# Performance work log

Measured on AMD Instinct MI355X. Metric: run time of the kernel, lower is better.

The kernel has to match this reference:

```python
import jax, jax.numpy as jnp
import numpy as np

EMB = 384
HID = 256
HEADS = 4
HD = HID // HEADS  # 64
LAYERS = 2
M_DOCS = 32
TOTAL = 4096  # 1 query + 32 docs + 4063 sentences
LN_EPS = 1e-5


def _layernorm(x, scale, bias):
    mu = jnp.mean(x, axis=-1, keepdims=True)
    var = jnp.mean(jnp.square(x - mu), axis=-1, keepdims=True)
    return (x - mu) * jax.lax.rsqrt(var + LN_EPS) * scale + bias


def setup_inputs() -> dict:
    key = jax.random.key(0)
    ks = jax.random.split(key, 12)
    g = 0.05  # small init scale (stand-in for xavier)
    return {
        "node_embeddings": jax.random.normal(ks[0], (TOTAL, EMB), jnp.float32),
        "adj": jax.random.randint(ks[1], (TOTAL, TOTAL), 0, 2, jnp.int32),
        "num_docs": M_DOCS,
        "proj_w": jax.random.normal(ks[2], (HID, EMB), jnp.float32) * g,
        "proj_b": jnp.zeros((HID,), jnp.float32),
        "ln_scale": jnp.ones((LAYERS, HID), jnp.float32),
        "ln_bias": jnp.zeros((LAYERS, HID), jnp.float32),
        "gat_W": jax.random.normal(ks[3], (LAYERS, HEADS, HD, HID), jnp.float32) * g,
        "gat_a": jax.random.normal(ks[4], (LAYERS, HEADS, 2 * HD), jnp.float32) * g,
        "fusion_w": jax.random.normal(ks[5], (HID, 2 * HID + 2), jnp.float32) * g,
        "fusion_b": jnp.zeros((HID,), jnp.float32),
        "out_w": jax.random.normal(ks[6], (HID,), jnp.float32) * g,
        "out_b": jnp.float32(0.5),
    }


def reference(node_embeddings, adj, num_docs, proj_w, proj_b, ln_scale, ln_bias,
              gat_W, gat_a, fusion_w, fusion_b, out_w, out_b):
    T = node_embeddings.shape[0]
    M = num_docs
    N = T - 1 - M  # number of sentences
    # input projection + relu (dropout = identity in eval)
    h = jax.nn.relu(node_embeddings @ proj_w.T + proj_b)  # (T, HID)
    # query-guided sentence re-weighting
    q = h[0:1]                     # (1, HID)
    s = h[1 + M:]                  # (N, HID)
    qn = q / (jnp.linalg.norm(q, axis=1, keepdims=True) + 1e-8)
    sn = s / (jnp.linalg.norm(s, axis=1, keepdims=True) + 1e-8)
    cos = (qn @ sn.T).reshape(-1, 1)          # (N,1)
    s = s + 0.8 * q * cos
    h = jnp.concatenate([h[:1 + M], s], axis=0)
    mask = (adj == 0)[None]                   # (1,T,T)
    for i in range(LAYERS):
        res = h
        x = _layernorm(h, ln_scale[i], ln_bias[i])
        Wh = jnp.einsum('nd,hkd->hnk', x, gat_W[i])                # (H,T,HD)
        # concat-attention a.[Wh_i ; Wh_j] == a_src.Wh_i + a_dst.Wh_j
        src = jnp.einsum('hnk,hk->hn', Wh, gat_a[i, :, :HD])       # (H,T)
        dst = jnp.einsum('hnk,hk->hn', Wh, gat_a[i, :, HD:])       # (H,T)
        e = jax.nn.leaky_relu(src[:, :, None] + dst[:, None, :], 0.2)  # (H,T,T)
        e = jnp.where(mask, -jnp.inf, e)
        attn = jax.nn.softmax(e, axis=-1)                          # softmax over j
        hn = jnp.einsum('hij,hjk->hik', attn, Wh)                  # (H,T,HD)
        hcat = jnp.transpose(hn, (1, 0, 2)).reshape(T, HEADS * HD)
        h = 0.5 * jax.nn.relu(hcat) + 0.5 * res
    qh = h[0:1]
    sh = h[1 + M:]
    scores = (qh @ sh.T) / (HID ** 0.5)       # (1,N)
    aw = jax.nn.softmax(scores, axis=-1)
    awT = aw.T                                # (N,1)
    qw = qh * (awT + 0.5)                     # (N,HID)
    qnf = qh / (jnp.linalg.norm(qh, axis=1, keepdims=True) + 1e-8)
    snf = sh / (jnp.linalg.norm(sh, axis=1, keepdims=True) + 1e-8)
    cosf = (qnf @ snf.T).reshape(-1, 1)       # (N,1)
    feat = jnp.concatenate([sh, qw, cosf, awT], axis=1)  # (N, 2*HID+2)
    g = jax.nn.relu(feat @ fusion_w.T + fusion_b)
    out = g @ out_w + out_b                   # (N,)
    return out + 0.5 * cosf[:, 0]
```

## Files before the change

kernel.cpp:

```cpp
#include <hip/hip_runtime.h>
#include <hip/hip_bf16.h>
#include <stdint.h>

#define TOTAL 4096
#define EMB 384
#define MD 32
#define NDOCS (TOTAL - 1 - MD)
#define LN_EPS 1e-5f

typedef __hip_bfloat16 bf16;
typedef unsigned short ushort_t;
typedef __attribute__((ext_vector_type(8))) short short8;
typedef __attribute__((ext_vector_type(4))) float f32x4;
typedef __attribute__((ext_vector_type(2))) float f32x2;

__device__ __forceinline__ float ldf(const void* p, int i, int isbf) {
    return isbf ? __bfloat162float(((const bf16*)p)[i]) : ((const float*)p)[i];
}

__device__ __forceinline__ ushort_t f2bf(float x) {
    return (ushort_t)((__float_as_uint(x) + 0x8000u) >> 16);
}

__global__ void k_detect(const uint16_t* p, int* flag) {
    __shared__ int red[4];
    int t = threadIdx.x;
    int cnt = 0;
    for (int k = t; k < 4096; k += 256) {
        uint16_t w = p[2 * k];
        int e = (w >> 7) & 0xFF;
        if (e >= 100 && e <= 140) cnt++;
    }
    for (int o = 32; o > 0; o >>= 1) cnt += __shfl_down(cnt, o);
    if ((t & 63) == 0) red[t >> 6] = cnt;
    __syncthreads();
    if (t == 0) flag[0] = (red[0] + red[1] + red[2] + red[3] > 2048) ? 1 : 0;
}

__global__ void k_transpose(const void* proj_w, const void* gat_W, const void* fusion_w,
                            float* projT, float* gatT, float* fwT, const int* flagp) {
    int isbf = flagp[0];
    int idx = blockIdx.x * 256 + threadIdx.x;
    if (idx < EMB * 256) {
        int d = idx >> 8, c = idx & 255;
        projT[idx] = ldf(proj_w, c * EMB + d, isbf);
    } else if (idx < EMB * 256 + 2 * 256 * 256) {
        int r = idx - EMB * 256;
        int l = r >> 16; int rem = r & 65535;
        int d = rem >> 8, c = rem & 255;
        gatT[r] = ldf(gat_W, l * 65536 + c * 256 + d, isbf);
    } else if (idx < EMB * 256 + 2 * 256 * 256 + 514 * 256) {
        int r = idx - (EMB * 256 + 2 * 256 * 256);
        int j = r >> 8, c = r & 255;
        fwT[r] = ldf(fusion_w, c * 514 + j, isbf);
    }
}

__global__ void k_adjmask(const int* adj, unsigned long long* maskb) {
    int i = blockIdx.x;
    int t = threadIdx.x;
    int w = t >> 6, l = t & 63;
    for (int c = w; c < 64; c += 4) {
        int a = adj[(size_t)i * TOTAL + c * 64 + l];
        unsigned long long m = __ballot(a != 0);
        if (l == 0) maskb[i * 64 + c] = m;
    }
}

#define PR 8
__global__ void k_proj(const void* emb, const void* proj_b, const float* projT, float* h,
                       const int* flagp) {
    __shared__ float xs[PR][EMB];
    int isbf = flagp[0];
    int i0 = blockIdx.x * PR, t = threadIdx.x;
    for (int idx = t; idx < PR * EMB; idx += 256) {
        int r = idx / EMB, d = idx % EMB;
        xs[r][d] = ldf(emb, (i0 + r) * EMB + d, isbf);
    }
    __syncthreads();
    float acc[PR];
    float bias = ldf(proj_b, t, isbf);
#pragma unroll
    for (int r = 0; r < PR; r++) acc[r] = bias;
    for (int d0 = 0; d0 < EMB; d0 += 4) {
        float w0 = projT[d0 * 256 + t];
        float w1 = projT[(d0 + 1) * 256 + t];
        float w2 = projT[(d0 + 2) * 256 + t];
        float w3 = projT[(d0 + 3) * 256 + t];
#pragma unroll
        for (int r = 0; r < PR; r++) {
            float4 x = *(const float4*)&xs[r][d0];
            acc[r] = fmaf(x.x, w0, acc[r]);
            acc[r] = fmaf(x.y, w1, acc[r]);
            acc[r] = fmaf(x.z, w2, acc[r]);
            acc[r] = fmaf(x.w, w3, acc[r]);
        }
    }
#pragma unroll
    for (int r = 0; r < PR; r++) h[(size_t)(i0 + r) * 256 + t] = fmaxf(acc[r], 0.f);
}

__global__ __launch_bounds__(256) void k_cosupdate(float* h) {
    int t = threadIdx.x, W = t >> 6, lane = t & 63;
    float4* h4 = (float4*)h;
    float4 q4 = h4[lane];
    float a = q4.x * q4.x + q4.y * q4.y + q4.z * q4.z + q4.w * q4.w;
    for (int o = 32; o > 0; o >>= 1) a += __shfl_xor(a, o);
    float qn = sqrtf(a) + 1e-8f;
    int gw = blockIdx.x * 4 + W;
    for (int n = gw; n < NDOCS; n += 1024) {
        size_t ro = (size_t)(1 + MD + n) * 64;
        float4 s4 = h4[ro + lane];
        float b = s4.x * s4.x + s4.y * s4.y + s4.z * s4.z + s4.w * s4.w;
        float c = q4.x * s4.x + q4.y * s4.y + q4.z * s4.z + q4.w * s4.w;
        for (int o = 32; o > 0; o >>= 1) { b += __shfl_xor(b, o); c += __shfl_xor(c, o); }
        float k = 0.8f * (c / (qn * (sqrtf(b) + 1e-8f)));
        s4.x += k * q4.x; s4.y += k * q4.y; s4.z += k * q4.z; s4.w += k * q4.w;
        h4[ro + lane] = s4;
    }
}

#define LR 4
__global__ void k_ln_wh(const float* h, const float* gatT, const void* ln_scale,
                        const void* ln_bias, const void* gat_a,
                        ushort_t* whswz, float* srcb, float* dstb, float* d1g, float* d2g,
                        int layer, const int* flagp) {
    __shared__ float xs[LR][256];
    __shared__ float red[2][LR][4];
    int isbf = flagp[0];
    int i0 = blockIdx.x * LR, t = threadIdx.x;
    int w = t >> 6, l = t & 63;
    float scale = ldf(ln_scale, layer * 256 + t, isbf);
    float bias = ldf(ln_bias, layer * 256 + t, isbf);
    float hv[LR];
#pragma unroll
    for (int r = 0; r < LR; r++) hv[r] = h[(size_t)(i0 + r) * 256 + t];
#pragma unroll
    for (int r = 0; r < LR; r++) {
        float a = hv[r], b = hv[r] * hv[r];
        for (int o = 32; o > 0; o >>= 1) { a += __shfl_down(a, o); b += __shfl_down(b, o); }
        if (l == 0) { red[0][r][w] = a; red[1][r][w] = b; }
    }
    __syncthreads();
#pragma unroll
    for (int r = 0; r < LR; r++) {
        float mu = (red[0][r][0] + red[0][r][1] + red[0][r][2] + red[0][r][3]) * (1.f / 256.f);
        float var = (red[1][r][0] + red[1][r][1] + red[1][r][2] + red[1][r][3]) * (1.f / 256.f) - mu * mu;
        float x = (hv[r] - mu) * rsqrtf(var + LN_EPS) * scale + bias;
        xs[r][t] = x;
    }
    __syncthreads();
    const float* gT = gatT + layer * 65536;
    float acc[LR] = {0.f, 0.f, 0.f, 0.f};
    for (int d0 = 0; d0 < 256; d0 += 4) {
        float w0 = gT[d0 * 256 + t];
        float w1 = gT[(d0 + 1) * 256 + t];
        float w2 = gT[(d0 + 2) * 256 + t];
        float w3 = gT[(d0 + 3) * 256 + t];
#pragma unroll
        for (int r = 0; r < LR; r++) {
            float4 x = *(const float4*)&xs[r][d0];
            acc[r] = fmaf(x.x, w0, acc[r]);
            acc[r] = fmaf(x.y, w1, acc[r]);
            acc[r] = fmaf(x.z, w2, acc[r]);
            acc[r] = fmaf(x.w, w3, acc[r]);
        }
    }
    float av1 = ldf(gat_a, layer * 512 + w * 128 + l, isbf);
    float av2 = ldf(gat_a, layer * 512 + w * 128 + 64 + l, isbf);
    const float LOG2E = 1.44269504f;
#pragma unroll
    for (int r = 0; r < LR; r++) {
        int i = i0 + r;
        int off = (i >> 6) * 16384 + (t >> 6) * 4096 + ((i >> 3) & 7) * 512 +
                  ((t >> 4) & 3) * 128 + (t & 15) * 8 + (i & 7);
        whswz[off] = f2bf(acc[r]);
        float sv = acc[r] * av1, dv = acc[r] * av2;
        for (int o = 32; o > 0; o >>= 1) { sv += __shfl_down(sv, o); dv += __shfl_down(dv, o); }
        if (l == 0) {
            srcb[w * 4096 + i] = sv;
            dstb[w * 4096 + i] = dv;
            d1g[w * 4096 + i] = dv * LOG2E;
            d2g[w * 4096 + i] = 0.2f * dv * LOG2E;
        }
    }
}

__global__ void k_dmax(const float* dstb, float* dmax) {
    __shared__ float red[4];
    int h = blockIdx.x, t = threadIdx.x;
    float m = -__builtin_inff();
    for (int j = t; j < 4096; j += 256) m = fmaxf(m, dstb[h * 4096 + j]);
    for (int o = 32; o > 0; o >>= 1) m = fmaxf(m, __shfl_down(m, o));
    if ((t & 63) == 0) red[t >> 6] = m;
    __syncthreads();
    if (t == 0) dmax[h] = fmaxf(fmaxf(red[0], red[1]), fmaxf(red[2], red[3]));
}

#define TI 32
#define JS 4
__global__ __launch_bounds__(512) void k_pv(const ushort_t* whswz, const float* srcb,
                                            const float* dmax, const float* d1g,
                                            const float* d2g,
                                            const unsigned long long* maskb,
                                            float* hnp, float* lpart) {
    __shared__ unsigned long long mbs[TI][17];
    __shared__ float d1s[4][1024];
    __shared__ float d2s[4][1024];
    __shared__ float srcs[4][TI], rces[4][TI];
    __shared__ unsigned int mlut[4];
    __shared__ __align__(16) float lsh[4][2][4][4];
    f32x4* accsh = (f32x4*)d1s;
    int t = threadIdx.x;
    int W = t >> 6, lane = t & 63;
    int h = W & 3, kq = W >> 2;
    int quad = lane >> 4, c16 = lane & 15;
    int i0 = blockIdx.x * TI;
    int jbase = blockIdx.y * 1024;
    if (t < 4) mlut[t] = (t & 1 ? 0x0000FFFFu : 0u) | (t & 2 ? 0xFFFF0000u : 0u);
    for (int idx = t; idx < TI * 16; idx += 512) {
        int r = idx >> 4, wd = idx & 15;
        mbs[r][wd] = maskb[(size_t)(i0 + r) * 64 + (jbase >> 6) + wd];
    }
    for (int idx = t; idx < 1024; idx += 512) {
        int hh = idx >> 8, j4 = idx & 255;
        ((float4*)d1s)[idx] = ((const float4*)(d1g + hh * 4096 + jbase))[j4];
        ((float4*)d2s)[idx] = ((const float4*)(d2g + hh * 4096 + jbase))[j4];
    }
    if (t < 128) {
        int h2 = t >> 5, r = t & 31;
        float sv = srcb[h2 * 4096 + i0 + r];
        srcs[h2][r] = sv;
        float sd = sv + dmax[h2];
        rces[h2][r] = -fmaxf(sd, 0.2f * sd);
    }
    __syncthreads();
    const float LOG2E = 1.44269504f;
    float s1[2], s2[2];
#pragma unroll
    for (int rt = 0; rt < 2; rt++) {
        float src = srcs[h][rt * 16 + c16], rce = rces[h][rt * 16 + c16];
        s1[rt] = (src + rce) * LOG2E;
        s2[rt] = (0.2f * src + rce) * LOG2E;
    }
    f32x4 acc[2][4];
    f32x4 accl[2] = {(f32x4){0.f, 0.f, 0.f, 0.f}, (f32x4){0.f, 0.f, 0.f, 0.f}};
#pragma unroll
    for (int rt = 0; rt < 2; rt++)
#pragma unroll
        for (int ct = 0; ct < 4; ct++) acc[rt][ct] = (f32x4){0.f, 0.f, 0.f, 0.f};
    uint4 onesu;
    unsigned os = (c16 == 0) ? 0x3F803F80u : 0u;
    onesu.x = os; onesu.y = os; onesu.z = os; onesu.w = os;
    short8 bfones = __builtin_bit_cast(short8, onesu);
    const uint4* g4 = (const uint4*)whswz;
    size_t b0 = (size_t)(jbase >> 6) * 2048 + h * 512 + (kq * 4 + quad) * 64 + c16;
    uint4 bn[4];
#pragma unroll
    for (int ct = 0; ct < 4; ct++) bn[ct] = g4[b0 + ct * 16];
    for (int step = 0; step < 16; step++) {
        uint4 bc[4];
#pragma unroll
        for (int ct = 0; ct < 4; ct++) bc[ct] = bn[ct];
        if (step < 15) {
            size_t bs = b0 + (size_t)(step + 1) * 2048;
#pragma unroll
            for (int ct = 0; ct < 4; ct++) bn[ct] = g4[bs + ct * 16];
        }
        int jl0 = step * 64 + kq * 32 + quad * 8;
        unsigned int mby[2];
#pragma unroll
        for (int rt = 0; rt < 2; rt++)
            mby[rt] = (unsigned int)(mbs[rt * 16 + c16][step] >> (kq * 32 + quad * 8)) & 0xFFu;
        const f32x2* p1 = (const f32x2*)&d1s[h][jl0];
        const f32x2* p2 = (const f32x2*)&d2s[h][jl0];
        f32x2 d1v[4] = {p1[0], p1[1], p1[2], p1[3]};
        f32x2 d2v[4] = {p2[0], p2[1], p2[2], p2[3]};
        uint4 afu[2];
#pragma unroll
        for (int rt = 0; rt < 2; rt++) {
            unsigned pu[4];
#pragma unroll
            for (int q = 0; q < 4; q++) {
                f32x2 t1 = d1v[q] + s1[rt];
                f32x2 t2 = d2v[q] + s2[rt];
                f32x2 m = __builtin_elementwise_max(t1, t2);
                float ea = exp2f(m.x), eb = exp2f(m.y);
                unsigned v = ((__float_as_uint(ea) + 0x8000u) >> 16) |
                             ((__float_as_uint(eb) + 0x8000u) & 0xFFFF0000u);
                pu[q] = v & mlut[(mby[rt] >> (2 * q)) & 3u];
            }
            afu[rt].x = pu[0]; afu[rt].y = pu[1]; afu[rt].z = pu[2]; afu[rt].w = pu[3];
        }
        short8 af0 = __builtin_bit_cast(short8, afu[0]);
        short8 af1 = __builtin_bit_cast(short8, afu[1]);
#pragma unroll
        for (int ct = 0; ct < 4; ct++) {
            short8 bf = __builtin_bit_cast(short8, bc[ct]);
            acc[0][ct] = __builtin_amdgcn_mfma_f32_16x16x32_bf16(af0, bf, acc[0][ct], 0, 0, 0);
            acc[1][ct] = __builtin_amdgcn_mfma_f32_16x16x32_bf16(af1, bf, acc[1][ct], 0, 0, 0);
        }
        accl[0] = __builtin_amdgcn_mfma_f32_16x16x32_bf16(af0, bfones, accl[0], 0, 0, 0);
        accl[1] = __builtin_amdgcn_mfma_f32_16x16x32_bf16(af1, bfones, accl[1], 0, 0, 0);
    }
    __syncthreads();
    if (kq == 1) {
#pragma unroll
        for (int rt = 0; rt < 2; rt++) {
#pragma unroll
            for (int ct = 0; ct < 4; ct++)
                accsh[((h * 2 + rt) * 4 + ct) * 64 + lane] = acc[rt][ct];
            if (c16 == 0) *(f32x4*)&lsh[h][rt][quad][0] = accl[rt];
        }
    }
    __syncthreads();
    if (kq == 0) {
        float* out = hnp + (size_t)blockIdx.y * (TOTAL * 256);
#pragma unroll
        for (int rt = 0; rt < 2; rt++) {
#pragma unroll
            for (int ct = 0; ct < 4; ct++) {
                f32x4 o = acc[rt][ct] + accsh[((h * 2 + rt) * 4 + ct) * 64 + lane];
#pragma unroll
                for (int rr = 0; rr < 4; rr++) {
                    int row = i0 + rt * 16 + quad * 4 + rr;
                    out[(size_t)row * 256 + h * 64 + ct * 16 + c16] = o[rr];
                }
            }
            if (c16 == 0) {
                f32x4 lv = accl[rt] + *(const f32x4*)&lsh[h][rt][quad][0];
#pragma unroll
                for (int rr = 0; rr < 4; rr++)
                    lpart[(size_t)(blockIdx.y * 4 + h) * 4096 + i0 + rt * 16 + quad * 4 + rr] = lv[rr];
            }
        }
    }
}

__global__ void k_epilogue(const float* hnp, const float* lpart, float* h) {
    int idx = blockIdx.x * 256 + threadIdx.x;
    int row = idx >> 6, hh_ = (idx >> 4) & 3;
    float l = 0.f;
#pragma unroll
    for (int js = 0; js < 4; js++)
        l += lpart[(size_t)(js * 4 + hh_) * 4096 + row];
    float inv = 1.f / l;
    const float4* p0 = (const float4*)hnp;
    const float4* p1 = (const float4*)(hnp + (size_t)TOTAL * 256);
    const float4* p2 = (const float4*)(hnp + (size_t)2 * TOTAL * 256);
    const float4* p3 = (const float4*)(hnp + (size_t)3 * TOTAL * 256);
    float4* h4 = (float4*)h;
    float4 a = p0[idx], b = p1[idx], c = p2[idx], d = p3[idx], hh = h4[idx];
    hh.x = 0.5f * fmaxf((a.x + b.x + c.x + d.x) * inv, 0.f) + 0.5f * hh.x;
    hh.y = 0.5f * fmaxf((a.y + b.y + c.y + d.y) * inv, 0.f) + 0.5f * hh.y;
    hh.z = 0.5f * fmaxf((a.z + b.z + c.z + d.z) * inv, 0.f) + 0.5f * hh.z;
    hh.w = 0.5f * fmaxf((a.w + b.w + c.w + d.w) * inv, 0.f) + 0.5f * hh.w;
    h4[idx] = hh;
}

__global__ __launch_bounds__(256) void k_scores(const float* h, float* scoresv, float* cosv) {
    int t = threadIdx.x, W = t >> 6, lane = t & 63;
    const float4* h4 = (const float4*)h;
    float4 q4 = h4[lane];
    float a = q4.x * q4.x + q4.y * q4.y + q4.z * q4.z + q4.w * q4.w;
    for (int o = 32; o > 0; o >>= 1) a += __shfl_xor(a, o);
    float qn = sqrtf(a) + 1e-8f;
    int gw = blockIdx.x * 4 + W;
    for (int n = gw; n < NDOCS; n += 1024) {
        size_t ro = (size_t)(1 + MD + n) * 64;
        float4 s4 = h4[ro + lane];
        float b = s4.x * s4.x + s4.y * s4.y + s4.z * s4.z + s4.w * s4.w;
        float c = q4.x * s4.x + q4.y * s4.y + q4.z * s4.z + q4.w * s4.w;
        for (int o = 32; o > 0; o >>= 1) { b += __shfl_xor(b, o); c += __shfl_xor(c, o); }
        if (lane == 0) {
            scoresv[n] = c * (1.f / 16.f);
            cosv[n] = c / (qn * (sqrtf(b) + 1e-8f));
        }
    }
}

__global__ __launch_bounds__(1024) void k_softmax(const float* scoresv, float* awv) {
    __shared__ float red[16];
    int t = threadIdx.x;
    float m = -__builtin_inff();
    for (int n = t; n < NDOCS; n += 1024) m = fmaxf(m, scoresv[n]);
    for (int o = 32; o > 0; o >>= 1) m = fmaxf(m, __shfl_down(m, o));
    if ((t & 63) == 0) red[t >> 6] = m;
    __syncthreads();
    m = red[0];
#pragma unroll
    for (int i = 1; i < 16; i++) m = fmaxf(m, red[i]);
    __syncthreads();
    float s = 0.f;
    for (int n = t; n < NDOCS; n += 1024) s += __expf(scoresv[n] - m);
    for (int o = 32; o > 0; o >>= 1) s += __shfl_down(s, o);
    if ((t & 63) == 0) red[t >> 6] = s;
    __syncthreads();
    s = 0.f;
#pragma unroll
    for (int i = 0; i < 16; i++) s += red[i];
    float inv = 1.f / s;
    for (int n = t; n < NDOCS; n += 1024) awv[n] = __expf(scoresv[n] - m) * inv;
}

#define TN 8
__global__ __launch_bounds__(256) void k_fusion(const float* h, const float* awv,
                                                const float* cosv, const float* fwT,
                                                const void* fusion_b, const void* out_w,
                                                const void* out_bp, void* outv,
                                                const int* flagp) {
    __shared__ float feats2[514][TN];
    __shared__ float qhs[256];
    __shared__ float red[TN][4];
    int isbf = flagp[0];
    int t = threadIdx.x;
    int n0 = blockIdx.x * TN;
    qhs[t] = h[t];
    __syncthreads();
    for (int idx = t; idx < 514 * TN; idx += 256) {
        int j = idx >> 3, r = idx & 7;
        int n = n0 + r;
        float v = 0.f;
        if (n < NDOCS) {
            if (j < 256) v = h[(size_t)(1 + MD + n) * 256 + j];
            else if (j < 512) v = qhs[j - 256] * (awv[n] + 0.5f);
            else if (j == 512) v = cosv[n];
            else v = awv[n];
        }
        feats2[j][r] = v;
    }
    __syncthreads();
    float acc[TN];
    float bk = ldf(fusion_b, t, isbf);
#pragma unroll
    for (int r = 0; r < TN; r++) acc[r] = bk;
    for (int j0 = 0; j0 < 512; j0 += 8) {
        float wv[8];
#pragma unroll
        for (int u = 0; u < 8; u++) wv[u] = fwT[(j0 + u) * 256 + t];
#pragma unroll
        for (int u = 0; u < 8; u++) {
            float4 a = *(const float4*)&feats2[j0 + u][0];
            float4 b = *(const float4*)&feats2[j0 + u][4];
            acc[0] = fmaf(a.x, wv[u], acc[0]);
            acc[1] = fmaf(a.y, wv[u], acc[1]);
            acc[2] = fmaf(a.z, wv[u], acc[2]);
            acc[3] = fmaf(a.w, wv[u], acc[3]);
            acc[4] = fmaf(b.x, wv[u], acc[4]);
            acc[5] = fmaf(b.y, wv[u], acc[5]);
            acc[6] = fmaf(b.z, wv[u], acc[6]);
            acc[7] = fmaf(b.w, wv[u], acc[7]);
        }
    }
#pragma unroll
    for (int j = 512; j < 514; j++) {
        float wv = fwT[j * 256 + t];
#pragma unroll
        for (int r = 0; r < TN; r++) acc[r] = fmaf(feats2[j][r], wv, acc[r]);
    }
    float ow = ldf(out_w, t, isbf);
    float outb = ldf(out_bp, 0, isbf);
#pragma unroll
    for (int r = 0; r < TN; r++) {
        float o = fmaxf(acc[r], 0.f) * ow;
        for (int off = 32; off > 0; off >>= 1) o += __shfl_down(o, off);
        if ((t & 63) == 0) red[r][t >> 6] = o;
    }
    __syncthreads();
    if (t < TN) {
        int n = n0 + t;
        if (n < NDOCS) {
            float o = red[t][0] + red[t][1] + red[t][2] + red[t][3] + outb + 0.5f * cosv[n];
            if (isbf) ((bf16*)outv)[n] = __float2bfloat16(o);
            else      ((float*)outv)[n] = o;
        }
    }
}

extern "C" void kernel_launch(void* const* d_in, const int* in_sizes, int n_in,
                              void* d_out, int out_size, void* d_ws, size_t ws_size,
                              hipStream_t stream) {
    const void* emb      = d_in[0];
    const int*  adj      = (const int*)d_in[1];
    const void* proj_w   = d_in[3];
    const void* proj_b   = d_in[4];
    const void* ln_scale = d_in[5];
    const void* ln_bias  = d_in[6];
    const void* gat_W    = d_in[7];
    const void* gat_a    = d_in[8];
    const void* fusion_w = d_in[9];
    const void* fusion_b = d_in[10];
    const void* out_w    = d_in[11];
    const void* out_b    = d_in[12];

    unsigned long long* maskb = (unsigned long long*)d_ws;
    int* flag = (int*)((char*)d_ws + (size_t)4096 * 64 * 8);
    float* f = (float*)((char*)d_ws + (size_t)4096 * 64 * 8 + 256);
    float* h       = f; f += 4096 * 256;
    float* srcb    = f; f += 4 * 4096;
    float* dstb    = f; f += 4 * 4096;
    float* d1g     = f; f += 4 * 4096;
    float* d2g     = f; f += 4 * 4096;
    float* dmax    = f; f += 64;
    float* projT   = f; f += EMB * 256;
    float* gatT    = f; f += 2 * 256 * 256;
    float* fwT     = f; f += 514 * 256;
    float* scoresv = f; f += 4096;
    float* cosv    = f; f += 4096;
    float* awv     = f; f += 4096;
    float* lpart   = f; f += 4 * 4 * 4096;
    ushort_t* whswz = (ushort_t*)f; f += 4096 * 256 / 2;
    float* hnp     = f; f += (size_t)JS * 4096 * 256;

    k_detect<<<dim3(1), dim3(256), 0, stream>>>((const uint16_t*)emb, flag);
    k_transpose<<<dim3(1410), dim3(256), 0, stream>>>(proj_w, gat_W, fusion_w, projT, gatT, fwT, flag);
    k_adjmask<<<dim3(4096), dim3(256), 0, stream>>>(adj, maskb);
    k_proj<<<dim3(TOTAL / PR), dim3(256), 0, stream>>>(emb, proj_b, projT, h, flag);
    k_cosupdate<<<dim3(256), dim3(256), 0, stream>>>(h);
    for (int layer = 0; layer < 2; layer++) {
        k_ln_wh<<<dim3(TOTAL / LR), dim3(256), 0, stream>>>(h, gatT, ln_scale, ln_bias, gat_a,
                                                            whswz, srcb, dstb, d1g, d2g, layer, flag);
        k_dmax<<<dim3(4), dim3(256), 0, stream>>>(dstb, dmax);
        k_pv<<<dim3(TOTAL / TI, JS), dim3(512), 0, stream>>>(whswz, srcb, dmax, d1g, d2g,
                                                             maskb, hnp, lpart);
        k_epilogue<<<dim3(1024), dim3(256), 0, stream>>>(hnp, lpart, h);
    }
    k_scores<<<dim3(256), dim3(256), 0, stream>>>(h, scoresv, cosv);
    k_softmax<<<dim3(1), dim3(1024), 0, stream>>>(scoresv, awv);
    k_fusion<<<dim3((NDOCS + TN - 1) / TN), dim3(256), 0, stream>>>(h, awv, cosv, fwT,
                                                                    fusion_b, out_w, out_b,
                                                                    (void*)d_out, flag);
}
```

Measured before the change: 342.6 us.

## Fuse epilogue, dmax, detect and transposes into neighbouring kernels; factor exp out of attention

```diff
diff --git a/kernel.cpp b/kernel.cpp
--- a/kernel.cpp
+++ b/kernel.cpp
@@ -18,45 +18,21 @@
     return isbf ? __bfloat162float(((const bf16*)p)[i]) : ((const float*)p)[i];
 }
 
-__device__ __forceinline__ ushort_t f2bf(float x) {
-    return (ushort_t)((__float_as_uint(x) + 0x8000u) >> 16);
-}
-
-__global__ void k_detect(const uint16_t* p, int* flag) {
+__device__ __forceinline__ unsigned f2bf(float x) {
+    return (__float_as_uint(x) + 0x8000u) >> 16;
+}
+
+__device__ __forceinline__ unsigned fenc(float f) {
+    unsigned u = __float_as_uint(f);
+    return (u >> 31) ? ~u : (u | 0x80000000u);
+}
+__device__ __forceinline__ float fdec(unsigned k) {
+    return __uint_as_float((k & 0x80000000u) ? (k & 0x7FFFFFFFu) : ~k);
+}
+
+__global__ void k_adjmask(const int* adj, unsigned long long* maskb,
+                          const uint16_t* embp, int* flag, unsigned* dmaxu) {
     __shared__ int red[4];
-    int t = threadIdx.x;
-    int cnt = 0;
-    for (int k = t; k < 4096; k += 256) {
-        uint16_t w = p[2 * k];
-        int e = (w >> 7) & 0xFF;
-        if (e >= 100 && e <= 140) cnt++;
-    }
-    for (int o = 32; o > 0; o >>= 1) cnt += __shfl_down(cnt, o);
-    if ((t & 63) == 0) red[t >> 6] = cnt;
-    __syncthreads();
-    if (t == 0) flag[0] = (red[0] + red[1] + red[2] + red[3] > 2048) ? 1 : 0;
-}
-
-__global__ void k_transpose(const void* proj_w, const void* gat_W, const void* fusion_w,
-                            float* projT, float* gatT, float* fwT, const int* flagp) {
-    int isbf = flagp[0];
-    int idx = blockIdx.x * 256 + threadIdx.x;
-    if (idx < EMB * 256) {
-        int d = idx >> 8, c = idx & 255;
-        projT[idx] = ldf(proj_w, c * EMB + d, isbf);
-    } else if (idx < EMB * 256 + 2 * 256 * 256) {
-        int r = idx - EMB * 256;
-        int l = r >> 16; int rem = r & 65535;
-        int d = rem >> 8, c = rem & 255;
-        gatT[r] = ldf(gat_W, l * 65536 + c * 256 + d, isbf);
-    } else if (idx < EMB * 256 + 2 * 256 * 256 + 514 * 256) {
-        int r = idx - (EMB * 256 + 2 * 256 * 256);
-        int j = r >> 8, c = r & 255;
-        fwT[r] = ldf(fusion_w, c * 514 + j, isbf);
-    }
-}
-
-__global__ void k_adjmask(const int* adj, unsigned long long* maskb) {
     int i = blockIdx.x;
     int t = threadIdx.x;
     int w = t >> 6, l = t & 63;
@@ -65,11 +41,24 @@
         unsigned long long m = __ballot(a != 0);
         if (l == 0) maskb[i * 64 + c] = m;
     }
+    if (i == 0) {
+        if (t < 8) dmaxu[t] = 0x007FFFFFu;
+        int cnt = 0;
+        for (int k = t; k < 4096; k += 256) {
+            uint16_t wd = embp[2 * k];
+            int e = (wd >> 7) & 0xFF;
+            if (e >= 100 && e <= 140) cnt++;
+        }
+        for (int o = 32; o > 0; o >>= 1) cnt += __shfl_down(cnt, o);
+        if ((t & 63) == 0) red[t >> 6] = cnt;
+        __syncthreads();
+        if (t == 0) flag[0] = (red[0] + red[1] + red[2] + red[3] > 2048) ? 1 : 0;
+    }
 }
 
 #define PR 8
-__global__ void k_proj(const void* emb, const void* proj_b, const float* projT, float* h,
-                       const int* flagp) {
+__global__ void k_proj(const void* emb, const void* proj_w, const void* proj_b,
+                       float* h, const int* flagp) {
     __shared__ float xs[PR][EMB];
     int isbf = flagp[0];
     int i0 = blockIdx.x * PR, t = threadIdx.x;
@@ -82,18 +71,41 @@
     float bias = ldf(proj_b, t, isbf);
 #pragma unroll
     for (int r = 0; r < PR; r++) acc[r] = bias;
-    for (int d0 = 0; d0 < EMB; d0 += 4) {
-        float w0 = projT[d0 * 256 + t];
-        float w1 = projT[(d0 + 1) * 256 + t];
-        float w2 = projT[(d0 + 2) * 256 + t];
-        float w3 = projT[(d0 + 3) * 256 + t];
-#pragma unroll
-        for (int r = 0; r < PR; r++) {
-            float4 x = *(const float4*)&xs[r][d0];
-            acc[r] = fmaf(x.x, w0, acc[r]);
-            acc[r] = fmaf(x.y, w1, acc[r]);
-            acc[r] = fmaf(x.z, w2, acc[r]);
-            acc[r] = fmaf(x.w, w3, acc[r]);
+    if (isbf) {
+        const uint4* pw = (const uint4*)((const ushort_t*)proj_w + (size_t)t * EMB);
+        for (int c = 0; c < EMB / 8; c++) {
+            uint4 u = pw[c];
+            float wv[8] = {
+                __uint_as_float(u.x << 16), __uint_as_float(u.x & 0xFFFF0000u),
+                __uint_as_float(u.y << 16), __uint_as_float(u.y & 0xFFFF0000u),
+                __uint_as_float(u.z << 16), __uint_as_float(u.z & 0xFFFF0000u),
+                __uint_as_float(u.w << 16), __uint_as_float(u.w & 0xFFFF0000u)};
+            int d0 = c * 8;
+#pragma unroll
+            for (int r = 0; r < PR; r++) {
+                float4 a = *(const float4*)&xs[r][d0];
+                float4 b = *(const float4*)&xs[r][d0 + 4];
+                acc[r] = fmaf(a.x, wv[0], acc[r]); acc[r] = fmaf(a.y, wv[1], acc[r]);
+                acc[r] = fmaf(a.z, wv[2], acc[r]); acc[r] = fmaf(a.w, wv[3], acc[r]);
+                acc[r] = fmaf(b.x, wv[4], acc[r]); acc[r] = fmaf(b.y, wv[5], acc[r]);
+                acc[r] = fmaf(b.z, wv[6], acc[r]); acc[r] = fmaf(b.w, wv[7], acc[r]);
+            }
+        }
+    } else {
+        const float4* pw = (const float4*)((const float*)proj_w + (size_t)t * EMB);
+        for (int c = 0; c < EMB / 8; c++) {
+            float4 wa = pw[2 * c], wb = pw[2 * c + 1];
+            float wv[8] = {wa.x, wa.y, wa.z, wa.w, wb.x, wb.y, wb.z, wb.w};
+            int d0 = c * 8;
+#pragma unroll
+            for (int r = 0; r < PR; r++) {
+                float4 a = *(const float4*)&xs[r][d0];
+                float4 b = *(const float4*)&xs[r][d0 + 4];
+                acc[r] = fmaf(a.x, wv[0], acc[r]); acc[r] = fmaf(a.y, wv[1], acc[r]);
+                acc[r] = fmaf(a.z, wv[2], acc[r]); acc[r] = fmaf(a.w, wv[3], acc[r]);
+                acc[r] = fmaf(b.x, wv[4], acc[r]); acc[r] = fmaf(b.y, wv[5], acc[r]);
+                acc[r] = fmaf(b.z, wv[6], acc[r]); acc[r] = fmaf(b.w, wv[7], acc[r]);
+            }
         }
     }
 #pragma unroll
@@ -121,10 +133,11 @@
 }
 
 #define LR 4
-__global__ void k_ln_wh(const float* h, const float* gatT, const void* ln_scale,
+__global__ void k_ln_wh(float* h, const void* gat_W, const void* ln_scale,
                         const void* ln_bias, const void* gat_a,
-                        ushort_t* whswz, float* srcb, float* dstb, float* d1g, float* d2g,
-                        int layer, const int* flagp) {
+                        ushort_t* whswz, float* srcb, unsigned* d12g, unsigned* dmaxu,
+                        const float* hnp, const float* lpart, int layer, int doepi,
+                        const int* flagp) {
     __shared__ float xs[LR][256];
     __shared__ float red[2][LR][4];
     int isbf = flagp[0];
@@ -133,8 +146,23 @@
     float scale = ldf(ln_scale, layer * 256 + t, isbf);
     float bias = ldf(ln_bias, layer * 256 + t, isbf);
     float hv[LR];
-#pragma unroll
-    for (int r = 0; r < LR; r++) hv[r] = h[(size_t)(i0 + r) * 256 + t];
+    if (doepi) {
+#pragma unroll
+        for (int r = 0; r < LR; r++) {
+            int i = i0 + r;
+            float lsum = lpart[(size_t)w * 4096 + i] + lpart[(size_t)(4 + w) * 4096 + i] +
+                         lpart[(size_t)(8 + w) * 4096 + i] + lpart[(size_t)(12 + w) * 4096 + i];
+            float s = hnp[(size_t)i * 256 + t] + hnp[(size_t)TOTAL * 256 + i * 256 + t] +
+                      hnp[(size_t)2 * TOTAL * 256 + i * 256 + t] +
+                      hnp[(size_t)3 * TOTAL * 256 + i * 256 + t];
+            float hn = 0.5f * fmaxf(s / lsum, 0.f) + 0.5f * h[(size_t)i * 256 + t];
+            hv[r] = hn;
+            h[(size_t)i * 256 + t] = hn;
+        }
+    } else {
+#pragma unroll
+        for (int r = 0; r < LR; r++) hv[r] = h[(size_t)(i0 + r) * 256 + t];
+    }
 #pragma unroll
     for (int r = 0; r < LR; r++) {
         float a = hv[r], b = hv[r] * hv[r];
@@ -150,67 +178,81 @@
         xs[r][t] = x;
     }
     __syncthreads();
-    const float* gT = gatT + layer * 65536;
+    size_t wbase = (size_t)layer * 65536 + (size_t)(t >> 6) * 16384 + (size_t)(t & 63) * 256;
     float acc[LR] = {0.f, 0.f, 0.f, 0.f};
-    for (int d0 = 0; d0 < 256; d0 += 4) {
-        float w0 = gT[d0 * 256 + t];
-        float w1 = gT[(d0 + 1) * 256 + t];
-        float w2 = gT[(d0 + 2) * 256 + t];
-        float w3 = gT[(d0 + 3) * 256 + t];
-#pragma unroll
-        for (int r = 0; r < LR; r++) {
-            float4 x = *(const float4*)&xs[r][d0];
-            acc[r] = fmaf(x.x, w0, acc[r]);
-            acc[r] = fmaf(x.y, w1, acc[r]);
-            acc[r] = fmaf(x.z, w2, acc[r]);
-            acc[r] = fmaf(x.w, w3, acc[r]);
+    if (isbf) {
+        const uint4* gw = (const uint4*)((const ushort_t*)gat_W + wbase);
+        for (int c = 0; c < 32; c++) {
+            uint4 u = gw[c];
+            float wv[8] = {
+                __uint_as_float(u.x << 16), __uint_as_float(u.x & 0xFFFF0000u),
+                __uint_as_float(u.y << 16), __uint_as_float(u.y & 0xFFFF0000u),
+                __uint_as_float(u.z << 16), __uint_as_float(u.z & 0xFFFF0000u),
+                __uint_as_float(u.w << 16), __uint_as_float(u.w & 0xFFFF0000u)};
+            int d0 = c * 8;
+#pragma unroll
+            for (int r = 0; r < LR; r++) {
+                float4 a = *(const float4*)&xs[r][d0];
+                float4 b = *(const float4*)&xs[r][d0 + 4];
+                acc[r] = fmaf(a.x, wv[0], acc[r]); acc[r] = fmaf(a.y, wv[1], acc[r]);
+                acc[r] = fmaf(a.z, wv[2], acc[r]); acc[r] = fmaf(a.w, wv[3], acc[r]);
+                acc[r] = fmaf(b.x, wv[4], acc[r]); acc[r] = fmaf(b.y, wv[5], acc[r]);
+                acc[r] = fmaf(b.z, wv[6], acc[r]); acc[r] = fmaf(b.w, wv[7], acc[r]);
+            }
+        }
+    } else {
+        const float4* gw = (const float4*)((const float*)gat_W + wbase);
+        for (int c = 0; c < 32; c++) {
+            float4 wa = gw[2 * c], wb = gw[2 * c + 1];
+            float wv[8] = {wa.x, wa.y, wa.z, wa.w, wb.x, wb.y, wb.z, wb.w};
+            int d0 = c * 8;
+#pragma unroll
+            for (int r = 0; r < LR; r++) {
+                float4 a = *(const float4*)&xs[r][d0];
+                float4 b = *(const float4*)&xs[r][d0 + 4];
+                acc[r] = fmaf(a.x, wv[0], acc[r]); acc[r] = fmaf(a.y, wv[1], acc[r]);
+                acc[r] = fmaf(a.z, wv[2], acc[r]); acc[r] = fmaf(a.w, wv[3], acc[r]);
+                acc[r] = fmaf(b.x, wv[4], acc[r]); acc[r] = fmaf(b.y, wv[5], acc[r]);
+                acc[r] = fmaf(b.z, wv[6], acc[r]); acc[r] = fmaf(b.w, wv[7], acc[r]);
+            }
         }
     }
     float av1 = ldf(gat_a, layer * 512 + w * 128 + l, isbf);
     float av2 = ldf(gat_a, layer * 512 + w * 128 + 64 + l, isbf);
     const float LOG2E = 1.44269504f;
+    float mmax = -__builtin_inff();
 #pragma unroll
     for (int r = 0; r < LR; r++) {
         int i = i0 + r;
         int off = (i >> 6) * 16384 + (t >> 6) * 4096 + ((i >> 3) & 7) * 512 +
                   ((t >> 4) & 3) * 128 + (t & 15) * 8 + (i & 7);
-        whswz[off] = f2bf(acc[r]);
+        whswz[off] = (ushort_t)f2bf(acc[r]);
         float sv = acc[r] * av1, dv = acc[r] * av2;
         for (int o = 32; o > 0; o >>= 1) { sv += __shfl_down(sv, o); dv += __shfl_down(dv, o); }
         if (l == 0) {
             srcb[w * 4096 + i] = sv;
-            dstb[w * 4096 + i] = dv;
-            d1g[w * 4096 + i] = dv * LOG2E;
-            d2g[w * 4096 + i] = 0.2f * dv * LOG2E;
-        }
-    }
-}
-
-__global__ void k_dmax(const float* dstb, float* dmax) {
-    __shared__ float red[4];
-    int h = blockIdx.x, t = threadIdx.x;
-    float m = -__builtin_inff();
-    for (int j = t; j < 4096; j += 256) m = fmaxf(m, dstb[h * 4096 + j]);
-    for (int o = 32; o > 0; o >>= 1) m = fmaxf(m, __shfl_down(m, o));
-    if ((t & 63) == 0) red[t >> 6] = m;
-    __syncthreads();
-    if (t == 0) dmax[h] = fmaxf(fmaxf(red[0], red[1]), fmaxf(red[2], red[3]));
+            float D1 = exp2f(dv * LOG2E), D2 = exp2f(0.2f * dv * LOG2E);
+            d12g[w * 4096 + i] = (f2bf(D2) << 16) | f2bf(D1);
+            mmax = fmaxf(mmax, dv);
+        }
+    }
+    if (l == 0) atomicMax(&dmaxu[w], fenc(mmax));
 }
 
 #define TI 32
 #define JS 4
 __global__ __launch_bounds__(512) void k_pv(const ushort_t* whswz, const float* srcb,
-                                            const float* dmax, const float* d1g,
-                                            const float* d2g,
+                                            const unsigned* dmaxu, const unsigned* d12g,
                                             const unsigned long long* maskb,
                                             float* hnp, float* lpart) {
-    __shared__ unsigned long long mbs[TI][17];
-    __shared__ float d1s[4][1024];
-    __shared__ float d2s[4][1024];
-    __shared__ float srcs[4][TI], rces[4][TI];
-    __shared__ unsigned int mlut[4];
+    __shared__ __align__(16) char smem[32768];
     __shared__ __align__(16) float lsh[4][2][4][4];
-    f32x4* accsh = (f32x4*)d1s;
+    __shared__ unsigned mlut[4];
+    unsigned* d12s = (unsigned*)smem;
+    unsigned long long* mbs = (unsigned long long*)(smem + 16384);
+    float* srcs = (float*)(smem + 16384 + 4352);
+    float* rces = srcs + 128;
+    f32x4* accsh = (f32x4*)smem;
     int t = threadIdx.x;
     int W = t >> 6, lane = t & 63;
     int h = W & 3, kq = W >> 2;
@@ -220,28 +262,28 @@
     if (t < 4) mlut[t] = (t & 1 ? 0x0000FFFFu : 0u) | (t & 2 ? 0xFFFF0000u : 0u);
     for (int idx = t; idx < TI * 16; idx += 512) {
         int r = idx >> 4, wd = idx & 15;
-        mbs[r][wd] = maskb[(size_t)(i0 + r) * 64 + (jbase >> 6) + wd];
+        mbs[r * 17 + wd] = maskb[(size_t)(i0 + r) * 64 + (jbase >> 6) + wd];
     }
     for (int idx = t; idx < 1024; idx += 512) {
         int hh = idx >> 8, j4 = idx & 255;
-        ((float4*)d1s)[idx] = ((const float4*)(d1g + hh * 4096 + jbase))[j4];
-        ((float4*)d2s)[idx] = ((const float4*)(d2g + hh * 4096 + jbase))[j4];
+        ((uint4*)d12s)[idx] = ((const uint4*)(d12g + hh * 4096 + jbase))[j4];
     }
     if (t < 128) {
         int h2 = t >> 5, r = t & 31;
         float sv = srcb[h2 * 4096 + i0 + r];
-        srcs[h2][r] = sv;
-        float sd = sv + dmax[h2];
-        rces[h2][r] = -fmaxf(sd, 0.2f * sd);
+        srcs[h2 * 32 + r] = sv;
+        float dm = fdec(dmaxu[h2]);
+        float sd = sv + dm;
+        rces[h2 * 32 + r] = -fmaxf(sd, 0.2f * sd);
     }
     __syncthreads();
     const float LOG2E = 1.44269504f;
-    float s1[2], s2[2];
+    float E1[2], E2[2];
 #pragma unroll
     for (int rt = 0; rt < 2; rt++) {
-        float src = srcs[h][rt * 16 + c16], rce = rces[h][rt * 16 + c16];
-        s1[rt] = (src + rce) * LOG2E;
-        s2[rt] = (0.2f * src + rce) * LOG2E;
+        float src = srcs[h * 32 + rt * 16 + c16], rce = rces[h * 32 + rt * 16 + c16];
+        E1[rt] = exp2f((src + rce) * LOG2E);
+        E2[rt] = exp2f((0.2f * src + rce) * LOG2E);
     }
     f32x4 acc[2][4];
     f32x4 accl[2] = {(f32x4){0.f, 0.f, 0.f, 0.f}, (f32x4){0.f, 0.f, 0.f, 0.f}};
@@ -268,26 +310,31 @@
             for (int ct = 0; ct < 4; ct++) bn[ct] = g4[bs + ct * 16];
         }
         int jl0 = step * 64 + kq * 32 + quad * 8;
-        unsigned int mby[2];
+        unsigned mby[2];
 #pragma unroll
         for (int rt = 0; rt < 2; rt++)
-            mby[rt] = (unsigned int)(mbs[rt * 16 + c16][step] >> (kq * 32 + quad * 8)) & 0xFFu;
-        const f32x2* p1 = (const f32x2*)&d1s[h][jl0];
-        const f32x2* p2 = (const f32x2*)&d2s[h][jl0];
-        f32x2 d1v[4] = {p1[0], p1[1], p1[2], p1[3]};
-        f32x2 d2v[4] = {p2[0], p2[1], p2[2], p2[3]};
+            mby[rt] = (unsigned)(mbs[(rt * 16 + c16) * 17 + step] >> (kq * 32 + quad * 8)) & 0xFFu;
+        const uint4* dj = (const uint4*)&d12s[h * 1024 + jl0];
+        uint4 da = dj[0], db = dj[1];
+        unsigned dw[8] = {da.x, da.y, da.z, da.w, db.x, db.y, db.z, db.w};
+        f32x2 D1[4], D2[4];
+#pragma unroll
+        for (int q = 0; q < 4; q++) {
+            unsigned a = dw[2 * q], b = dw[2 * q + 1];
+            D1[q] = (f32x2){__uint_as_float(a << 16), __uint_as_float(b << 16)};
+            D2[q] = (f32x2){__uint_as_float(a & 0xFFFF0000u), __uint_as_float(b & 0xFFFF0000u)};
+        }
         uint4 afu[2];
 #pragma unroll
         for (int rt = 0; rt < 2; rt++) {
             unsigned pu[4];
 #pragma unroll
             for (int q = 0; q < 4; q++) {
-                f32x2 t1 = d1v[q] + s1[rt];
-                f32x2 t2 = d2v[q] + s2[rt];
-                f32x2 m = __builtin_elementwise_max(t1, t2);
-                float ea = exp2f(m.x), eb = exp2f(m.y);
-                unsigned v = ((__float_as_uint(ea) + 0x8000u) >> 16) |
-                             ((__float_as_uint(eb) + 0x8000u) & 0xFFFF0000u);
+                f32x2 v1 = D1[q] * E1[rt];
+                f32x2 v2 = D2[q] * E2[rt];
+                f32x2 m = __builtin_elementwise_max(v1, v2);
+                unsigned v = ((__float_as_uint(m.x) + 0x8000u) >> 16) |
+                             ((__float_as_uint(m.y) + 0x8000u) & 0xFFFF0000u);
                 pu[q] = v & mlut[(mby[rt] >> (2 * q)) & 3u];
             }
             afu[rt].x = pu[0]; afu[rt].y = pu[1]; afu[rt].z = pu[2]; afu[rt].w = pu[3];
@@ -337,38 +384,44 @@
     }
 }
 
-__global__ void k_epilogue(const float* hnp, const float* lpart, float* h) {
-    int idx = blockIdx.x * 256 + threadIdx.x;
-    int row = idx >> 6, hh_ = (idx >> 4) & 3;
-    float l = 0.f;
-#pragma unroll
-    for (int js = 0; js < 4; js++)
-        l += lpart[(size_t)(js * 4 + hh_) * 4096 + row];
-    float inv = 1.f / l;
+__global__ __launch_bounds__(256) void k_scores(float* h, const float* hnp, const float* lpart,
+                                                float* qrow, float* scoresv, float* cosv) {
+    int t = threadIdx.x, W = t >> 6, lane = t & 63;
+    int hh = lane >> 4;
+    float4* h4 = (float4*)h;
     const float4* p0 = (const float4*)hnp;
-    const float4* p1 = (const float4*)(hnp + (size_t)TOTAL * 256);
-    const float4* p2 = (const float4*)(hnp + (size_t)2 * TOTAL * 256);
-    const float4* p3 = (const float4*)(hnp + (size_t)3 * TOTAL * 256);
-    float4* h4 = (float4*)h;
-    float4 a = p0[idx], b = p1[idx], c = p2[idx], d = p3[idx], hh = h4[idx];
-    hh.x = 0.5f * fmaxf((a.x + b.x + c.x + d.x) * inv, 0.f) + 0.5f * hh.x;
-    hh.y = 0.5f * fmaxf((a.y + b.y + c.y + d.y) * inv, 0.f) + 0.5f * hh.y;
-    hh.z = 0.5f * fmaxf((a.z + b.z + c.z + d.z) * inv, 0.f) + 0.5f * hh.z;
-    hh.w = 0.5f * fmaxf((a.w + b.w + c.w + d.w) * inv, 0.f) + 0.5f * hh.w;
-    h4[idx] = hh;
-}
-
-__global__ __launch_bounds__(256) void k_scores(const float* h, float* scoresv, float* cosv) {
-    int t = threadIdx.x, W = t >> 6, lane = t & 63;
-    const float4* h4 = (const float4*)h;
-    float4 q4 = h4[lane];
+    const float4* p1 = p0 + (size_t)TOTAL * 64;
+    const float4* p2 = p1 + (size_t)TOTAL * 64;
+    const float4* p3 = p2 + (size_t)TOTAL * 64;
+    int gw = blockIdx.x * 4 + W;
+    float lq = lpart[(size_t)hh * 4096] + lpart[(size_t)(4 + hh) * 4096] +
+               lpart[(size_t)(8 + hh) * 4096] + lpart[(size_t)(12 + hh) * 4096];
+    float4 a0 = p0[lane], a1 = p1[lane], a2 = p2[lane], a3 = p3[lane];
+    float4 hq = h4[lane];
+    float invq = 1.f / lq;
+    float4 q4;
+    q4.x = 0.5f * fmaxf((a0.x + a1.x + a2.x + a3.x) * invq, 0.f) + 0.5f * hq.x;
+    q4.y = 0.5f * fmaxf((a0.y + a1.y + a2.y + a3.y) * invq, 0.f) + 0.5f * hq.y;
+    q4.z = 0.5f * fmaxf((a0.z + a1.z + a2.z + a3.z) * invq, 0.f) + 0.5f * hq.z;
+    q4.w = 0.5f * fmaxf((a0.w + a1.w + a2.w + a3.w) * invq, 0.f) + 0.5f * hq.w;
+    if (gw == 0) ((float4*)qrow)[lane] = q4;
     float a = q4.x * q4.x + q4.y * q4.y + q4.z * q4.z + q4.w * q4.w;
     for (int o = 32; o > 0; o >>= 1) a += __shfl_xor(a, o);
     float qn = sqrtf(a) + 1e-8f;
-    int gw = blockIdx.x * 4 + W;
     for (int n = gw; n < NDOCS; n += 1024) {
-        size_t ro = (size_t)(1 + MD + n) * 64;
-        float4 s4 = h4[ro + lane];
+        int row = 1 + MD + n;
+        size_t ro = (size_t)row * 64;
+        float ld = lpart[(size_t)hh * 4096 + row] + lpart[(size_t)(4 + hh) * 4096 + row] +
+                   lpart[(size_t)(8 + hh) * 4096 + row] + lpart[(size_t)(12 + hh) * 4096 + row];
+        float4 b0 = p0[ro + lane], b1 = p1[ro + lane], b2 = p2[ro + lane], b3 = p3[ro + lane];
+        float4 ho = h4[ro + lane];
+        float invd = 1.f / ld;
+        float4 s4;
+        s4.x = 0.5f * fmaxf((b0.x + b1.x + b2.x + b3.x) * invd, 0.f) + 0.5f * ho.x;
+        s4.y = 0.5f * fmaxf((b0.y + b1.y + b2.y + b3.y) * invd, 0.f) + 0.5f * ho.y;
+        s4.z = 0.5f * fmaxf((b0.z + b1.z + b2.z + b3.z) * invd, 0.f) + 0.5f * ho.z;
+        s4.w = 0.5f * fmaxf((b0.w + b1.w + b2.w + b3.w) * invd, 0.f) + 0.5f * ho.w;
+        h4[ro + lane] = s4;
         float b = s4.x * s4.x + s4.y * s4.y + s4.z * s4.z + s4.w * s4.w;
         float c = q4.x * s4.x + q4.y * s4.y + q4.z * s4.z + q4.w * s4.w;
         for (int o = 32; o > 0; o >>= 1) { b += __shfl_xor(b, o); c += __shfl_xor(c, o); }
@@ -404,18 +457,18 @@
 }
 
 #define TN 8
-__global__ __launch_bounds__(256) void k_fusion(const float* h, const float* awv,
-                                                const float* cosv, const float* fwT,
-                                                const void* fusion_b, const void* out_w,
-                                                const void* out_bp, void* outv,
-                                                const int* flagp) {
+__global__ __launch_bounds__(256) void k_fusion(const float* h, const float* qrow,
+                                                const float* awv, const float* cosv,
+                                                const void* fusion_w, const void* fusion_b,
+                                                const void* out_w, const void* out_bp,
+                                                void* outv, const int* flagp) {
     __shared__ float feats2[514][TN];
     __shared__ float qhs[256];
     __shared__ float red[TN][4];
     int isbf = flagp[0];
     int t = threadIdx.x;
     int n0 = blockIdx.x * TN;
-    qhs[t] = h[t];
+    qhs[t] = qrow[t];
     __syncthreads();
     for (int idx = t; idx < 514 * TN; idx += 256) {
         int j = idx >> 3, r = idx & 7;
@@ -434,27 +487,46 @@
     float bk = ldf(fusion_b, t, isbf);
 #pragma unroll
     for (int r = 0; r < TN; r++) acc[r] = bk;
-    for (int j0 = 0; j0 < 512; j0 += 8) {
-        float wv[8];
-#pragma unroll
-        for (int u = 0; u < 8; u++) wv[u] = fwT[(j0 + u) * 256 + t];
-#pragma unroll
-        for (int u = 0; u < 8; u++) {
-            float4 a = *(const float4*)&feats2[j0 + u][0];
-            float4 b = *(const float4*)&feats2[j0 + u][4];
-            acc[0] = fmaf(a.x, wv[u], acc[0]);
-            acc[1] = fmaf(a.y, wv[u], acc[1]);
-            acc[2] = fmaf(a.z, wv[u], acc[2]);
-            acc[3] = fmaf(a.w, wv[u], acc[3]);
-            acc[4] = fmaf(b.x, wv[u], acc[4]);
-            acc[5] = fmaf(b.y, wv[u], acc[5]);
-            acc[6] = fmaf(b.z, wv[u], acc[6]);
-            acc[7] = fmaf(b.w, wv[u], acc[7]);
+    if (isbf) {
+        const unsigned* pw = (const unsigned*)fusion_w + (size_t)t * 257;
+        for (int c = 0; c < 64; c++) {
+            unsigned u0 = pw[4 * c], u1 = pw[4 * c + 1], u2 = pw[4 * c + 2], u3 = pw[4 * c + 3];
+            float wv[8] = {
+                __uint_as_float(u0 << 16), __uint_as_float(u0 & 0xFFFF0000u),
+                __uint_as_float(u1 << 16), __uint_as_float(u1 & 0xFFFF0000u),
+                __uint_as_float(u2 << 16), __uint_as_float(u2 & 0xFFFF0000u),
+                __uint_as_float(u3 << 16), __uint_as_float(u3 & 0xFFFF0000u)};
+            int j0 = c * 8;
+#pragma unroll
+            for (int u = 0; u < 8; u++) {
+                float4 fa = *(const float4*)&feats2[j0 + u][0];
+                float4 fb = *(const float4*)&feats2[j0 + u][4];
+                acc[0] = fmaf(fa.x, wv[u], acc[0]); acc[1] = fmaf(fa.y, wv[u], acc[1]);
+                acc[2] = fmaf(fa.z, wv[u], acc[2]); acc[3] = fmaf(fa.w, wv[u], acc[3]);
+                acc[4] = fmaf(fb.x, wv[u], acc[4]); acc[5] = fmaf(fb.y, wv[u], acc[5]);
+                acc[6] = fmaf(fb.z, wv[u], acc[6]); acc[7] = fmaf(fb.w, wv[u], acc[7]);
+            }
+        }
+    } else {
+        const float2* pw = (const float2*)((const float*)fusion_w + (size_t)t * 514);
+        for (int c = 0; c < 64; c++) {
+            float2 w0 = pw[4 * c], w1 = pw[4 * c + 1], w2 = pw[4 * c + 2], w3 = pw[4 * c + 3];
+            float wv[8] = {w0.x, w0.y, w1.x, w1.y, w2.x, w2.y, w3.x, w3.y};
+            int j0 = c * 8;
+#pragma unroll
+            for (int u = 0; u < 8; u++) {
+                float4 fa = *(const float4*)&feats2[j0 + u][0];
+                float4 fb = *(const float4*)&feats2[j0 + u][4];
+                acc[0] = fmaf(fa.x, wv[u], acc[0]); acc[1] = fmaf(fa.y, wv[u], acc[1]);
+                acc[2] = fmaf(fa.z, wv[u], acc[2]); acc[3] = fmaf(fa.w, wv[u], acc[3]);
+                acc[4] = fmaf(fb.x, wv[u], acc[4]); acc[5] = fmaf(fb.y, wv[u], acc[5]);
+                acc[6] = fmaf(fb.z, wv[u], acc[6]); acc[7] = fmaf(fb.w, wv[u], acc[7]);
+            }
         }
     }
 #pragma unroll
     for (int j = 512; j < 514; j++) {
-        float wv = fwT[j * 256 + t];
+        float wv = ldf(fusion_w, t * 514 + j, isbf);
 #pragma unroll
         for (int r = 0; r < TN; r++) acc[r] = fmaf(feats2[j][r], wv, acc[r]);
     }
@@ -498,36 +570,29 @@
     float* f = (float*)((char*)d_ws + (size_t)4096 * 64 * 8 + 256);
     float* h       = f; f += 4096 * 256;
     float* srcb    = f; f += 4 * 4096;
-    float* dstb    = f; f += 4 * 4096;
-    float* d1g     = f; f += 4 * 4096;
-    float* d2g     = f; f += 4 * 4096;
-    float* dmax    = f; f += 64;
-    float* projT   = f; f += EMB * 256;
-    float* gatT    = f; f += 2 * 256 * 256;
-    float* fwT     = f; f += 514 * 256;
+    unsigned* d12g = (unsigned*)f; f += 4 * 4096;
+    unsigned* dmaxu = (unsigned*)f; f += 64;
     float* scoresv = f; f += 4096;
     float* cosv    = f; f += 4096;
     float* awv     = f; f += 4096;
+    float* qrow    = f; f += 256;
     float* lpart   = f; f += 4 * 4 * 4096;
     ushort_t* whswz = (ushort_t*)f; f += 4096 * 256 / 2;
     float* hnp     = f; f += (size_t)JS * 4096 * 256;
 
-    k_detect<<<dim3(1), dim3(256), 0, stream>>>((const uint16_t*)emb, flag);
-    k_transpose<<<dim3(1410), dim3(256), 0, stream>>>(proj_w, gat_W, fusion_w, projT, gatT, fwT, flag);
-    k_adjmask<<<dim3(4096), dim3(256), 0, stream>>>(adj, maskb);
-    k_proj<<<dim3(TOTAL / PR), dim3(256), 0, stream>>>(emb, proj_b, projT, h, flag);
+    k_adjmask<<<dim3(4096), dim3(256), 0, stream>>>(adj, maskb, (const uint16_t*)emb, flag, dmaxu);
+    k_proj<<<dim3(TOTAL / PR), dim3(256), 0, stream>>>(emb, proj_w, proj_b, h, flag);
     k_cosupdate<<<dim3(256), dim3(256), 0, stream>>>(h);
     for (int layer = 0; layer < 2; layer++) {
-        k_ln_wh<<<dim3(TOTAL / LR), dim3(256), 0, stream>>>(h, gatT, ln_scale, ln_bias, gat_a,
-                                                            whswz, srcb, dstb, d1g, d2g, layer, flag);
-        k_dmax<<<dim3(4), dim3(256), 0, stream>>>(dstb, dmax);
-        k_pv<<<dim3(TOTAL / TI, JS), dim3(512), 0, stream>>>(whswz, srcb, dmax, d1g, d2g,
-                                                             maskb, hnp, lpart);
-        k_epilogue<<<dim3(1024), dim3(256), 0, stream>>>(hnp, lpart, h);
-    }
-    k_scores<<<dim3(256), dim3(256), 0, stream>>>(h, scoresv, cosv);
+        k_ln_wh<<<dim3(TOTAL / LR), dim3(256), 0, stream>>>(h, gat_W, ln_scale, ln_bias, gat_a,
+                                                            whswz, srcb, d12g, dmaxu + layer * 4,
+                                                            hnp, lpart, layer, layer, flag);
+        k_pv<<<dim3(TOTAL / TI, JS), dim3(512), 0, stream>>>(whswz, srcb, dmaxu + layer * 4,
+                                                             d12g, maskb, hnp, lpart);
+    }
+    k_scores<<<dim3(256), dim3(256), 0, stream>>>(h, hnp, lpart, qrow, scoresv, cosv);
     k_softmax<<<dim3(1), dim3(1024), 0, stream>>>(scoresv, awv);
-    k_fusion<<<dim3((NDOCS + TN - 1) / TN), dim3(256), 0, stream>>>(h, awv, cosv, fwT,
-                                                                    fusion_b, out_w, out_b,
-                                                                    (void*)d_out, flag);
-}
+    k_fusion<<<dim3((NDOCS + TN - 1) / TN), dim3(256), 0, stream>>>(h, qrow, awv, cosv,
+                                                                    fusion_w, fusion_b, out_w,
+                                                                    out_b, (void*)d_out, flag);
+}
```

New measurement: 409.2 us. 19.4% more time.
